# Kernel tuning notes

Hardware: AMD Instinct MI355X
Metric: run time of the kernel (lower is better)

The kernel has to match this reference:

```python
import jax, jax.numpy as jnp
from jax import lax
import numpy as np

BS, T, C, N, K, D, H = 8, 32, 64, 4096, 32, 64, 64
NB, BSZ, NG, BPG = 4, 8, 1, 4  # dendritic tree: 4 branches of 8, 1 group of 4 branches


def setup_inputs() -> dict:
    key = jax.random.key(0)
    ks = jax.random.split(key, 16)
    fc1_scale = (2.0 / (5 * D + H)) ** 0.5
    return {
        "cc_signals": jax.random.normal(ks[0], (BS, T, C, D), jnp.float32),
        "h": jax.random.normal(ks[1], (BS, N, D), jnp.float32) * 0.1,
        "prev_messages": jnp.tanh(jax.random.normal(ks[2], (BS, N, D), jnp.float32)),
        "trace_prim": jax.random.normal(ks[3], (BS, N, D), jnp.float32) * 0.1,
        "trace_key": jax.random.normal(ks[4], (BS, N, D), jnp.float32) * 0.1,
        "primitives": jax.random.normal(ks[5], (N, D), jnp.float32),
        "key_p": jax.random.normal(ks[6], (N, D), jnp.float32),
        "decay_logit": jax.random.normal(ks[7], (N,), jnp.float32) * 0.1,
        "dendrite_branch_w": 1.0 / BSZ + jax.random.normal(ks[8], (N, NB, BSZ, D), jnp.float32) * 0.05,
        "dendrite_group_w": 1.0 / BPG + jax.random.normal(ks[9], (N, NG, BPG, D), jnp.float32) * 0.05,
        "fc1_w": jax.random.normal(ks[10], (N, 5 * D, H), jnp.float32) * fc1_scale,
        "fc1_b": jnp.zeros((N, H), jnp.float32),
        "fc2_w": jax.random.normal(ks[11], (N, H, 3), jnp.float32) * 0.05,
        "fc2_b": jnp.zeros((N, 3), jnp.float32),
        "mod_lr_logit": jnp.full((1,), -2.0, jnp.float32),
        "conn_indices": jax.random.randint(ks[12], (N, K), 0, N),
        "stride": 4,
    }


def reference(cc_signals, h, prev_messages, trace_prim, trace_key, primitives,
              key_p, decay_logit, dendrite_branch_w, dendrite_group_w,
              fc1_w, fc1_b, fc2_w, fc2_b, mod_lr_logit, conn_indices, stride):
    bsz, tseg, c, d = cc_signals.shape
    n = primitives.shape[0]
    k = conn_indices.shape[1]
    nb, bsize = dendrite_branch_w.shape[1], dendrite_branch_w.shape[2]
    ng, bpg = dendrite_group_w.shape[1], dendrite_group_w.shape[2]
    n_tree = ng * bpg * bsize

    # --- per-neuron modulator MLP (once per segment) ---
    prim_b = jnp.broadcast_to(primitives[None], (bsz, n, d))
    key_b = jnp.broadcast_to(key_p[None], (bsz, n, d))
    mod_input = jnp.concatenate([h, trace_prim, trace_key, prim_b, key_b], axis=-1)  # [B,N,5D]
    x = jnp.tanh(jnp.einsum('bnd,ndh->bnh', mod_input, fc1_w) + fc1_b)
    out = jnp.einsum('bnh,nho->bno', x, fc2_w) + fc2_b  # [B,N,3]
    gate_prim = jnp.tanh(out[..., 0:1])
    gate_key = jnp.tanh(out[..., 1:2])
    decay_mod = out[..., 2]

    mod_lr = jax.nn.sigmoid(mod_lr_logit[0])
    tp_dir = trace_prim / jnp.maximum(jnp.linalg.norm(trace_prim, axis=-1, keepdims=True), 1e-8)
    tk_dir = trace_key / jnp.maximum(jnp.linalg.norm(trace_key, axis=-1, keepdims=True), 1e-8)
    eff_prim = primitives[None] + mod_lr * gate_prim * tp_dir        # [B,N,D]
    eff_key = key_p[None] + mod_lr * gate_key * tk_dir               # [B,N,D]
    eff_decay = jax.nn.sigmoid(decay_logit[None] + decay_mod)[..., None]  # [B,N,1]

    def dendritic(weighted):  # weighted: [B,N,K,D]
        tree = weighted[:, :, :n_tree].reshape(bsz, n, nb, bsize, d)
        branch = jnp.tanh(jnp.sum(tree * dendrite_branch_w[None], axis=3))   # [B,N,nb,D]
        grouped = branch.reshape(bsz, n, ng, bpg, d)
        group = jnp.tanh(jnp.sum(grouped * dendrite_group_w[None], axis=3))  # [B,N,ng,D]
        received = group.mean(axis=2)
        if n_tree < k:  # static
            leftover = weighted[:, :, n_tree:].sum(axis=2)
            frac = n_tree / k
            received = frac * received + (1.0 - frac) * leftover
        return received

    def update(hh, pm, cc_t):
        nb_msgs = pm[:, conn_indices]                                # gather: [B,N,K,D]
        sim = jnp.einsum('bnd,bnkd->bnk', eff_key, nb_msgs)
        weighted = jax.nn.sigmoid(sim)[..., None] * nb_msgs
        received = dendritic(weighted)
        received = received.at[:, :c].add(cc_t)
        h2 = eff_decay * hh + (1.0 - eff_decay) * received
        return h2, jnp.tanh(h2 * eff_prim)

    def step(carry, inp):
        hh, pm = carry
        t, cc_t = inp
        hh, pm = lax.cond(t % stride == 0,
                          lambda a, b: update(a, b, cc_t),
                          lambda a, b: (a, b), hh, pm)
        return (hh, pm), pm[:, :c]

    ts = jnp.arange(tseg)
    cc_tfirst = jnp.transpose(cc_signals, (1, 0, 2, 3))  # [T,B,C,D]
    _, outs = lax.scan(step, (h, prev_messages), (ts, cc_tfirst))
    return jnp.transpose(outs, (1, 0, 2, 3))  # [B,T,C,D]
```

## Files before the change

kernel.cpp:

```cpp
#include <hip/hip_runtime.h>
#include <hip/hip_bf16.h>

#define BS 8
#define T_ 32
#define C_ 64
#define N_ 4096
#define K_ 32
#define D_ 64
#define H_ 64

typedef __hip_bfloat16 bf16;

__device__ __forceinline__ float fexp2(float x){ return __builtin_amdgcn_exp2f(x); }
__device__ __forceinline__ float frcp(float x){ return __builtin_amdgcn_rcpf(x); }
__device__ __forceinline__ float sigm(float x){ return frcp(1.f + fexp2(-1.44269504f*x)); }
__device__ __forceinline__ float tanh_(float x){ return 1.f - 2.f*frcp(1.f + fexp2(2.88539008f*x)); }

__device__ __forceinline__ float ld1(const bf16* p, int i){ return __bfloat162float(p[i]); }
__device__ __forceinline__ float ld1(const float* p, int i){ return p[i]; }
__device__ __forceinline__ void st1(bf16* p, int i, float v){ p[i] = __float2bfloat16(v); }
__device__ __forceinline__ void st1(float* p, int i, float v){ p[i] = v; }

__device__ __forceinline__ float rl(float x, int j){
  return __uint_as_float(__builtin_amdgcn_readlane(__float_as_uint(x), j));
}

__device__ __forceinline__ float allsum(float v){
  #pragma unroll
  for (int d = 1; d < 64; d <<= 1) v += __shfl_xor(v, d, 64);
  return v;
}

__device__ __forceinline__ bool is_bf16(const void* mll){
  return ((const unsigned short*)mll)[0] == 0xC000u;
}

template<typename TI>
__device__ __forceinline__ void mod_body(
    const TI* h_in, const TI* tp, const TI* tk, const TI* prim, const TI* keyp,
    const TI* dlog, const TI* w1, const TI* b1, const TI* w2, const TI* bb2, const TI* mll,
    float* cp_a, float* ck_a, float* dc_a, int n, int lane)
{
  float h_r[BS], tp_r[BS], tk_r[BS];
  #pragma unroll
  for (int b = 0; b < BS; b++){
    int src = (b*N_ + n)*D_ + lane;
    h_r[b]  = ld1(h_in, src);
    tp_r[b] = ld1(tp, src);
    tk_r[b] = ld1(tk, src);
  }
  float prim_r = ld1(prim, n*D_ + lane);
  float keyp_r = ld1(keyp, n*D_ + lane);

  const TI* wrow = w1 + n*(320*H_) + lane;
  float acc[BS] = {};
  float accs = 0.f;
  #pragma unroll 4
  for (int j = 0; j < 64; j++){
    float w0v = ld1(wrow, (      j)*H_);
    float w1v = ld1(wrow, ( 64 + j)*H_);
    float w2v = ld1(wrow, (128 + j)*H_);
    float w3v = ld1(wrow, (192 + j)*H_);
    float w4v = ld1(wrow, (256 + j)*H_);
    #pragma unroll
    for (int b = 0; b < BS; b++){
      acc[b] = fmaf(rl(h_r[b],  j), w0v, acc[b]);
      acc[b] = fmaf(rl(tp_r[b], j), w1v, acc[b]);
      acc[b] = fmaf(rl(tk_r[b], j), w2v, acc[b]);
    }
    accs = fmaf(rl(prim_r, j), w3v, accs);
    accs = fmaf(rl(keyp_r, j), w4v, accs);
  }

  float bb  = ld1(b1, n*H_ + lane);
  float w20 = ld1(w2, n*(H_*3) + lane*3 + 0);
  float w21 = ld1(w2, n*(H_*3) + lane*3 + 1);
  float w22 = ld1(w2, n*(H_*3) + lane*3 + 2);
  float bo0 = ld1(bb2, n*3 + 0);
  float bo1 = ld1(bb2, n*3 + 1);
  float bo2 = ld1(bb2, n*3 + 2);
  float mlr = sigm(ld1(mll, 0));
  float dl  = ld1(dlog, n);
  #pragma unroll
  for (int b = 0; b < BS; b++){
    float x  = tanh_(acc[b] + accs + bb);
    float o0 = allsum(x*w20) + bo0;
    float o1 = allsum(x*w21) + bo1;
    float o2 = allsum(x*w22) + bo2;
    float tpd = tp_r[b];
    float tkd = tk_r[b];
    float npn = fmaxf(sqrtf(allsum(tpd*tpd)), 1e-8f);
    float nkn = fmaxf(sqrtf(allsum(tkd*tkd)), 1e-8f);
    if (lane == 0){
      int g = b*N_ + n;
      cp_a[g] = mlr * tanh_(o0) * frcp(npn);
      ck_a[g] = mlr * tanh_(o1) * frcp(nkn);
      dc_a[g] = sigm(dl + o2);
    }
  }
}

__global__ __launch_bounds__(64) void k_mod(
    const void* h_in, const void* tp, const void* tk, const void* prim, const void* keyp,
    const void* dlog, const void* w1, const void* b1, const void* w2, const void* bb2,
    const void* mll, float* cp_a, float* ck_a, float* dc_a)
{
  int n = blockIdx.x, lane = threadIdx.x;
  if (is_bf16(mll))
    mod_body<bf16>((const bf16*)h_in,(const bf16*)tp,(const bf16*)tk,(const bf16*)prim,
                   (const bf16*)keyp,(const bf16*)dlog,(const bf16*)w1,(const bf16*)b1,
                   (const bf16*)w2,(const bf16*)bb2,(const bf16*)mll,
                   cp_a, ck_a, dc_a, n, lane);
  else
    mod_body<float>((const float*)h_in,(const float*)tp,(const float*)tk,(const float*)prim,
                    (const float*)keyp,(const float*)dlog,(const float*)w1,(const float*)b1,
                    (const float*)w2,(const float*)bb2,(const float*)mll,
                    cp_a, ck_a, dc_a, n, lane);
}

template<typename TH>
__global__ __launch_bounds__(256) void k_inith(const void* h_in, const void* mll, TH* h_ws){
  int i = blockIdx.x*256 + threadIdx.x;
  if (is_bf16(mll)) st1(h_ws, i, ld1((const bf16*)h_in, i));
  else              st1(h_ws, i, ld1((const float*)h_in, i));
}

template<typename TS>
__global__ __launch_bounds__(256) void k_initpm(const void* pm_in, const void* mll, TS* pm_ws){
  int i = blockIdx.x*256 + threadIdx.x;
  if (is_bf16(mll)) st1(pm_ws, i, ld1((const bf16*)pm_in, i));
  else              st1(pm_ws, i, ld1((const float*)pm_in, i));
}

template<typename TI, typename TS, typename TH>
__device__ __forceinline__ void step_body(
    const TS* pm_in, TS* pm_out, TH* h_ws,
    const float* cp_a, const float* ck_a, const float* dc_a,
    const TI* tp, const TI* tk, const TI* prim, const TI* keyp,
    const TI* dbw, const TI* dgw, const TI* cc, const int* conn,
    TI* out, int tcur)
{
  int lane = threadIdx.x & 63;
  int n    = blockIdx.x*4 + (threadIdx.x >> 6);

  int idxv = conn[n*K_ + (lane & 31)];
  float bw_r[K_];
  #pragma unroll
  for (int k = 0; k < K_; k++) bw_r[k] = ld1(dbw, n*(K_*D_) + k*D_ + lane);
  float gw_r[4];
  #pragma unroll
  for (int j = 0; j < 4; j++) gw_r[j] = ld1(dgw, n*(4*D_) + j*D_ + lane);
  float keyp_r = ld1(keyp, n*D_ + lane);
  float prim_r = ld1(prim, n*D_ + lane);

  #pragma unroll 1
  for (int b = 0; b < BS; b++){
    int g  = b*N_ + n;
    int rb = g*D_ + lane;
    float keyd = fmaf(ck_a[g], ld1(tk, rb), keyp_r);
    const TS* pmb = pm_in + (size_t)(b*N_)*D_ + lane;

    float msg[K_];
    #pragma unroll
    for (int k = 0; k < K_; k++){
      int m = __builtin_amdgcn_readlane(idxv, k);
      msg[k] = ld1(pmb, m*D_);
    }

    float r[16];
    {
      bool hb = (lane & 1) != 0;
      #pragma unroll
      for (int j = 0; j < 16; j++){
        float a  = keyd * msg[2*j];
        float bq = keyd * msg[2*j+1];
        float lo = hb ? bq : a;
        float hi = hb ? a  : bq;
        r[j] = lo + __shfl_xor(hi, 1, 64);
      }
    }
    #pragma unroll
    for (int s = 1; s < 5; s++){
      int m = 1 << s;
      bool hb = (lane & m) != 0;
      #pragma unroll
      for (int j = 0; j < (16 >> s); j++){
        float a  = r[2*j];
        float bq = r[2*j+1];
        float lo = hb ? bq : a;
        float hi = hb ? a  : bq;
        r[j] = lo + __shfl_xor(hi, m, 64);
      }
    }
    float simv = r[0] + __shfl_xor(r[0], 32, 64);
    float wv = sigm(simv);

    float accb[4] = {};
    #pragma unroll
    for (int k = 0; k < K_; k++){
      float w = rl(wv, k);
      accb[k>>3] = fmaf(w*msg[k], bw_r[k], accb[k>>3]);
    }

    float gg = 0.f;
    #pragma unroll
    for (int j = 0; j < 4; j++)
      gg = fmaf(tanh_(accb[j]), gw_r[j], gg);
    float recv = tanh_(gg);
    if (n < C_) recv += ld1(cc, ((b*T_ + tcur)*C_ + n)*D_ + lane);
    float dec = dc_a[g];
    float hv = ld1(h_ws, rb);
    float h2 = recv + dec*(hv - recv);
    st1(h_ws, rb, h2);
    float effp = fmaf(cp_a[g], ld1(tp, rb), prim_r);
    float pmv = tanh_(h2 * effp);
    st1(pm_out, rb, pmv);
    if (n < C_){
      #pragma unroll
      for (int dt = 0; dt < 4; dt++)
        st1(out, ((b*T_ + tcur + dt)*C_ + n)*D_ + lane, pmv);
    }
  }
}

template<typename TS, typename TH>
__global__ __launch_bounds__(256) void k_step(
    const TS* pm_in, TS* pm_out, TH* h_ws,
    const float* cp_a, const float* ck_a, const float* dc_a,
    const void* tp, const void* tk, const void* prim, const void* keyp,
    const void* dbw, const void* dgw, const void* cc, const int* conn,
    void* out, const void* mll, int tcur)
{
  if (is_bf16(mll))
    step_body<bf16,TS,TH>(pm_in, pm_out, h_ws, cp_a, ck_a, dc_a,
        (const bf16*)tp,(const bf16*)tk,(const bf16*)prim,(const bf16*)keyp,
        (const bf16*)dbw,(const bf16*)dgw,(const bf16*)cc, conn, (bf16*)out, tcur);
  else
    step_body<float,TS,TH>(pm_in, pm_out, h_ws, cp_a, ck_a, dc_a,
        (const float*)tp,(const float*)tk,(const float*)prim,(const float*)keyp,
        (const float*)dbw,(const float*)dgw,(const float*)cc, conn, (float*)out, tcur);
}

template<typename TS, typename TH>
static void launch_all(void* const* d_in, void* d_out, void* d_ws, hipStream_t stream)
{
  const void* cc   = d_in[0];
  const void* h_in = d_in[1];
  const void* pmsg = d_in[2];
  const void* tp   = d_in[3];
  const void* tk   = d_in[4];
  const void* prim = d_in[5];
  const void* keyp = d_in[6];
  const void* dlog = d_in[7];
  const void* dbw  = d_in[8];
  const void* dgw  = d_in[9];
  const void* w1   = d_in[10];
  const void* b1   = d_in[11];
  const void* w2   = d_in[12];
  const void* bb2  = d_in[13];
  const void* mll  = d_in[14];
  const int* conn  = (const int*)d_in[15];

  const int NE = BS*N_*D_;
  const int BSN = BS*N_;
  char* p = (char*)d_ws;
  TH* h_ws = (TH*)p;            p += (size_t)NE*sizeof(TH);
  float* cp_a = (float*)p;      p += (size_t)BSN*4;
  float* ck_a = (float*)p;      p += (size_t)BSN*4;
  float* dc_a = (float*)p;      p += (size_t)BSN*4;
  TS* pm0 = (TS*)p;             p += (size_t)NE*sizeof(TS);
  TS* pm1 = (TS*)p;

  k_inith<TH><<<NE/256, 256, 0, stream>>>(h_in, mll, h_ws);
  k_initpm<TS><<<NE/256, 256, 0, stream>>>(pmsg, mll, pm0);
  k_mod<<<N_, 64, 0, stream>>>(h_in, tp, tk, prim, keyp, dlog, w1, b1, w2, bb2, mll,
                               cp_a, ck_a, dc_a);
  for (int s = 0; s < 8; s++){
    const TS* pin = (s & 1) ? pm1 : pm0;
    TS* pout = (s & 1) ? pm0 : pm1;
    k_step<TS,TH><<<dim3(N_/4), 256, 0, stream>>>(
        pin, pout, h_ws, cp_a, ck_a, dc_a,
        tp, tk, prim, keyp, dbw, dgw, cc, conn, d_out, mll, 4*s);
  }
}

extern "C" void kernel_launch(void* const* d_in, const int* in_sizes, int n_in,
                              void* d_out, int out_size, void* d_ws, size_t ws_size,
                              hipStream_t stream)
{
  (void)in_sizes; (void)n_in; (void)out_size;
  const size_t NE = (size_t)BS*N_*D_;
  const size_t gates = 3ull*BS*N_*4;
  if (ws_size >= NE*4 + gates + 2*NE*4)
    launch_all<float, float>(d_in, d_out, d_ws, stream);
  else if (ws_size >= NE*4 + gates + 2*NE*2)
    launch_all<bf16, float>(d_in, d_out, d_ws, stream);
  else
    launch_all<bf16, bf16>(d_in, d_out, d_ws, stream);
}
```

Measured before the change: 917.0 us.

## Fuse step kernels into one persistent kernel with software grid barriers

Replaces the two init kernels and eight per-step launches with a single persistent kernel of 256 blocks × 512 threads. Neurons stay resident per block, with branch weights held in LDS and h, decay, key and prim terms kept in registers across steps. Steps are separated by atomic grid barriers. This removes launch gaps and repeated per-step reloads of per-neuron data. In exchange, all blocks must be co-resident or the barriers deadlock, and each step now runs on only 256 blocks, which may limit latency hiding on the gather.

```diff
diff --git a/kernel.cpp b/kernel.cpp
--- a/kernel.cpp
+++ b/kernel.cpp
@@ -8,6 +8,8 @@
 #define K_ 32
 #define D_ 64
 #define H_ 64
+#define NBLK 256
+#define NTHR 512
 
 typedef __hip_bfloat16 bf16;
 
@@ -118,130 +120,162 @@
                     cp_a, ck_a, dc_a, n, lane);
 }
 
-template<typename TH>
-__global__ __launch_bounds__(256) void k_inith(const void* h_in, const void* mll, TH* h_ws){
-  int i = blockIdx.x*256 + threadIdx.x;
-  if (is_bf16(mll)) st1(h_ws, i, ld1((const bf16*)h_in, i));
-  else              st1(h_ws, i, ld1((const float*)h_in, i));
-}
-
-template<typename TS>
-__global__ __launch_bounds__(256) void k_initpm(const void* pm_in, const void* mll, TS* pm_ws){
-  int i = blockIdx.x*256 + threadIdx.x;
-  if (is_bf16(mll)) st1(pm_ws, i, ld1((const bf16*)pm_in, i));
-  else              st1(pm_ws, i, ld1((const float*)pm_in, i));
-}
-
-template<typename TI, typename TS, typename TH>
-__device__ __forceinline__ void step_body(
-    const TS* pm_in, TS* pm_out, TH* h_ws,
+__global__ __launch_bounds__(64) void k_binit(unsigned* slots){
+  if (threadIdx.x < 16) slots[threadIdx.x] = 0u;
+}
+
+__device__ __forceinline__ void gridbar(unsigned* slot, int tid){
+  __threadfence();
+  __syncthreads();
+  if (tid == 0){
+    __hip_atomic_fetch_add(slot, 1u, __ATOMIC_ACQ_REL, __HIP_MEMORY_SCOPE_AGENT);
+    while (__hip_atomic_load(slot, __ATOMIC_ACQUIRE, __HIP_MEMORY_SCOPE_AGENT) < (unsigned)NBLK)
+      __builtin_amdgcn_s_sleep(1);
+  }
+  __syncthreads();
+  __threadfence();
+}
+
+template<typename TI, typename TS>
+__device__ __forceinline__ void fused_body(
+    const TI* h_in, const TI* pmsg,
     const float* cp_a, const float* ck_a, const float* dc_a,
     const TI* tp, const TI* tk, const TI* prim, const TI* keyp,
     const TI* dbw, const TI* dgw, const TI* cc, const int* conn,
-    TI* out, int tcur)
-{
-  int lane = threadIdx.x & 63;
-  int n    = blockIdx.x*4 + (threadIdx.x >> 6);
-
-  int idxv = conn[n*K_ + (lane & 31)];
-  float bw_r[K_];
+    TS* pm0, TS* pm1, unsigned* slots, TI* out, float* bwsh)
+{
+  int tid  = threadIdx.x;
+  int lane = tid & 63;
+  int w    = tid >> 6;
+  int nb   = blockIdx.x * 16;
+
+  {
+    int base = blockIdx.x*NTHR + tid;
+    #pragma unroll
+    for (int j = 0; j < 16; j++){
+      int idx = base + j*(NBLK*NTHR);
+      st1(pm0, idx, ld1(pmsg, idx));
+    }
+  }
+
+  int idxv[2];
+  float gw[2][4], keyd[2][BS], effp[2][BS], dec[2][BS], hreg[2][BS];
   #pragma unroll
-  for (int k = 0; k < K_; k++) bw_r[k] = ld1(dbw, n*(K_*D_) + k*D_ + lane);
-  float gw_r[4];
-  #pragma unroll
-  for (int j = 0; j < 4; j++) gw_r[j] = ld1(dgw, n*(4*D_) + j*D_ + lane);
-  float keyp_r = ld1(keyp, n*D_ + lane);
-  float prim_r = ld1(prim, n*D_ + lane);
+  for (int i = 0; i < 2; i++){
+    int n = nb + 2*w + i;
+    idxv[i] = conn[n*K_ + (lane & 31)];
+    #pragma unroll
+    for (int k = 0; k < K_; k++)
+      bwsh[((2*w+i)*K_ + k)*D_ + lane] = ld1(dbw, n*(K_*D_) + k*D_ + lane);
+    #pragma unroll
+    for (int j = 0; j < 4; j++)
+      gw[i][j] = ld1(dgw, n*(4*D_) + j*D_ + lane);
+    float kp = ld1(keyp, n*D_ + lane);
+    float pr = ld1(prim, n*D_ + lane);
+    #pragma unroll
+    for (int b = 0; b < BS; b++){
+      int g = b*N_ + n, rb = g*D_ + lane;
+      keyd[i][b] = fmaf(ck_a[g], ld1(tk, rb), kp);
+      effp[i][b] = fmaf(cp_a[g], ld1(tp, rb), pr);
+      dec[i][b]  = dc_a[g];
+      hreg[i][b] = ld1(h_in, rb);
+    }
+  }
+  gridbar(&slots[0], tid);
 
   #pragma unroll 1
-  for (int b = 0; b < BS; b++){
-    int g  = b*N_ + n;
-    int rb = g*D_ + lane;
-    float keyd = fmaf(ck_a[g], ld1(tk, rb), keyp_r);
-    const TS* pmb = pm_in + (size_t)(b*N_)*D_ + lane;
-
-    float msg[K_];
-    #pragma unroll
-    for (int k = 0; k < K_; k++){
-      int m = __builtin_amdgcn_readlane(idxv, k);
-      msg[k] = ld1(pmb, m*D_);
-    }
-
-    float r[16];
-    {
-      bool hb = (lane & 1) != 0;
+  for (int s = 0; s < 8; s++){
+    const TS* pA = (s & 1) ? pm1 : pm0;
+    TS*       pB = (s & 1) ? pm0 : pm1;
+    #pragma unroll
+    for (int i = 0; i < 2; i++){
+      int n = nb + 2*w + i;
       #pragma unroll
-      for (int j = 0; j < 16; j++){
-        float a  = keyd * msg[2*j];
-        float bq = keyd * msg[2*j+1];
-        float lo = hb ? bq : a;
-        float hi = hb ? a  : bq;
-        r[j] = lo + __shfl_xor(hi, 1, 64);
+      for (int b = 0; b < BS; b++){
+        const TS* pmb = pA + (size_t)(b*N_)*D_ + lane;
+        float msg[K_];
+        #pragma unroll
+        for (int k = 0; k < K_; k++){
+          int m = __builtin_amdgcn_readlane(idxv[i], k);
+          msg[k] = ld1(pmb, m*D_);
+        }
+        float r[16];
+        {
+          bool hb = (lane & 1) != 0;
+          #pragma unroll
+          for (int j = 0; j < 16; j++){
+            float a  = keyd[i][b] * msg[2*j];
+            float bq = keyd[i][b] * msg[2*j+1];
+            float lo = hb ? bq : a;
+            float hi = hb ? a  : bq;
+            r[j] = lo + __shfl_xor(hi, 1, 64);
+          }
+        }
+        #pragma unroll
+        for (int st = 1; st < 5; st++){
+          int m = 1 << st;
+          bool hb = (lane & m) != 0;
+          #pragma unroll
+          for (int j = 0; j < (16 >> st); j++){
+            float a  = r[2*j];
+            float bq = r[2*j+1];
+            float lo = hb ? bq : a;
+            float hi = hb ? a  : bq;
+            r[j] = lo + __shfl_xor(hi, m, 64);
+          }
+        }
+        float simv = r[0] + __shfl_xor(r[0], 32, 64);
+        float wv = sigm(simv);
+
+        float accb[4] = {};
+        #pragma unroll
+        for (int k = 0; k < K_; k++){
+          float wq = rl(wv, k);
+          accb[k>>3] = fmaf(wq*msg[k], bwsh[((2*w+i)*K_+k)*D_+lane], accb[k>>3]);
+        }
+        float gg = 0.f;
+        #pragma unroll
+        for (int j = 0; j < 4; j++)
+          gg = fmaf(tanh_(accb[j]), gw[i][j], gg);
+        float recv = tanh_(gg);
+        if (n < C_) recv += ld1(cc, ((b*T_ + 4*s)*C_ + n)*D_ + lane);
+        float h2 = recv + dec[i][b]*(hreg[i][b] - recv);
+        hreg[i][b] = h2;
+        float pmv = tanh_(h2 * effp[i][b]);
+        st1(pB, (b*N_ + n)*D_ + lane, pmv);
+        if (n < C_){
+          #pragma unroll
+          for (int dt = 0; dt < 4; dt++)
+            st1(out, ((b*T_ + 4*s + dt)*C_ + n)*D_ + lane, pmv);
+        }
       }
     }
-    #pragma unroll
-    for (int s = 1; s < 5; s++){
-      int m = 1 << s;
-      bool hb = (lane & m) != 0;
-      #pragma unroll
-      for (int j = 0; j < (16 >> s); j++){
-        float a  = r[2*j];
-        float bq = r[2*j+1];
-        float lo = hb ? bq : a;
-        float hi = hb ? a  : bq;
-        r[j] = lo + __shfl_xor(hi, m, 64);
-      }
-    }
-    float simv = r[0] + __shfl_xor(r[0], 32, 64);
-    float wv = sigm(simv);
-
-    float accb[4] = {};
-    #pragma unroll
-    for (int k = 0; k < K_; k++){
-      float w = rl(wv, k);
-      accb[k>>3] = fmaf(w*msg[k], bw_r[k], accb[k>>3]);
-    }
-
-    float gg = 0.f;
-    #pragma unroll
-    for (int j = 0; j < 4; j++)
-      gg = fmaf(tanh_(accb[j]), gw_r[j], gg);
-    float recv = tanh_(gg);
-    if (n < C_) recv += ld1(cc, ((b*T_ + tcur)*C_ + n)*D_ + lane);
-    float dec = dc_a[g];
-    float hv = ld1(h_ws, rb);
-    float h2 = recv + dec*(hv - recv);
-    st1(h_ws, rb, h2);
-    float effp = fmaf(cp_a[g], ld1(tp, rb), prim_r);
-    float pmv = tanh_(h2 * effp);
-    st1(pm_out, rb, pmv);
-    if (n < C_){
-      #pragma unroll
-      for (int dt = 0; dt < 4; dt++)
-        st1(out, ((b*T_ + tcur + dt)*C_ + n)*D_ + lane, pmv);
-    }
-  }
-}
-
-template<typename TS, typename TH>
-__global__ __launch_bounds__(256) void k_step(
-    const TS* pm_in, TS* pm_out, TH* h_ws,
+    if (s < 7) gridbar(&slots[s+1], tid);
+  }
+}
+
+template<typename TS>
+__global__ __launch_bounds__(NTHR, 2) void k_fused(
+    const void* h_in, const void* pmsg,
     const float* cp_a, const float* ck_a, const float* dc_a,
     const void* tp, const void* tk, const void* prim, const void* keyp,
     const void* dbw, const void* dgw, const void* cc, const int* conn,
-    void* out, const void* mll, int tcur)
-{
+    TS* pm0, TS* pm1, unsigned* slots, void* out, const void* mll)
+{
+  __shared__ float bwsh[16*K_*D_];
   if (is_bf16(mll))
-    step_body<bf16,TS,TH>(pm_in, pm_out, h_ws, cp_a, ck_a, dc_a,
+    fused_body<bf16,TS>((const bf16*)h_in,(const bf16*)pmsg, cp_a, ck_a, dc_a,
         (const bf16*)tp,(const bf16*)tk,(const bf16*)prim,(const bf16*)keyp,
-        (const bf16*)dbw,(const bf16*)dgw,(const bf16*)cc, conn, (bf16*)out, tcur);
+        (const bf16*)dbw,(const bf16*)dgw,(const bf16*)cc, conn,
+        pm0, pm1, slots, (bf16*)out, bwsh);
   else
-    step_body<float,TS,TH>(pm_in, pm_out, h_ws, cp_a, ck_a, dc_a,
+    fused_body<float,TS>((const float*)h_in,(const float*)pmsg, cp_a, ck_a, dc_a,
         (const float*)tp,(const float*)tk,(const float*)prim,(const float*)keyp,
-        (const float*)dbw,(const float*)dgw,(const float*)cc, conn, (float*)out, tcur);
-}
-
-template<typename TS, typename TH>
+        (const float*)dbw,(const float*)dgw,(const float*)cc, conn,
+        pm0, pm1, slots, (float*)out, bwsh);
+}
+
+template<typename TS>
 static void launch_all(void* const* d_in, void* d_out, void* d_ws, hipStream_t stream)
 {
   const void* cc   = d_in[0];
@@ -261,27 +295,22 @@
   const void* mll  = d_in[14];
   const int* conn  = (const int*)d_in[15];
 
-  const int NE = BS*N_*D_;
+  const int NE  = BS*N_*D_;
   const int BSN = BS*N_;
   char* p = (char*)d_ws;
-  TH* h_ws = (TH*)p;            p += (size_t)NE*sizeof(TH);
   float* cp_a = (float*)p;      p += (size_t)BSN*4;
   float* ck_a = (float*)p;      p += (size_t)BSN*4;
   float* dc_a = (float*)p;      p += (size_t)BSN*4;
+  unsigned* slots = (unsigned*)p; p += 256;
   TS* pm0 = (TS*)p;             p += (size_t)NE*sizeof(TS);
   TS* pm1 = (TS*)p;
 
-  k_inith<TH><<<NE/256, 256, 0, stream>>>(h_in, mll, h_ws);
-  k_initpm<TS><<<NE/256, 256, 0, stream>>>(pmsg, mll, pm0);
   k_mod<<<N_, 64, 0, stream>>>(h_in, tp, tk, prim, keyp, dlog, w1, b1, w2, bb2, mll,
                                cp_a, ck_a, dc_a);
-  for (int s = 0; s < 8; s++){
-    const TS* pin = (s & 1) ? pm1 : pm0;
-    TS* pout = (s & 1) ? pm0 : pm1;
-    k_step<TS,TH><<<dim3(N_/4), 256, 0, stream>>>(
-        pin, pout, h_ws, cp_a, ck_a, dc_a,
-        tp, tk, prim, keyp, dbw, dgw, cc, conn, d_out, mll, 4*s);
-  }
+  k_binit<<<1, 64, 0, stream>>>(slots);
+  k_fused<TS><<<NBLK, NTHR, 0, stream>>>(h_in, pmsg, cp_a, ck_a, dc_a,
+                                         tp, tk, prim, keyp, dbw, dgw, cc, conn,
+                                         pm0, pm1, slots, d_out, mll);
 }
 
 extern "C" void kernel_launch(void* const* d_in, const int* in_sizes, int n_in,
@@ -290,11 +319,9 @@
 {
   (void)in_sizes; (void)n_in; (void)out_size;
   const size_t NE = (size_t)BS*N_*D_;
-  const size_t gates = 3ull*BS*N_*4;
-  if (ws_size >= NE*4 + gates + 2*NE*4)
-    launch_all<float, float>(d_in, d_out, d_ws, stream);
-  else if (ws_size >= NE*4 + gates + 2*NE*2)
-    launch_all<bf16, float>(d_in, d_out, d_ws, stream);
+  const size_t head = 3ull*BS*N_*4 + 256;
+  if (ws_size >= head + 2*NE*4)
+    launch_all<float>(d_in, d_out, d_ws, stream);
   else
-    launch_all<bf16, bf16>(d_in, d_out, d_ws, stream);
-}
+    launch_all<bf16>(d_in, d_out, d_ws, stream);
+}
```

Measured after the change: 1.663 ms. +81.3%, slower.
